# Optimization experiments

Measured on AMD Instinct MI355X. Metric: run time of the kernel, lower is better.

## Reference

```python
import jax, jax.numpy as jnp
import numpy as np
import math

S = 3  # num_subset

def _pe(C, T, V, domain):
    # sinusoidal positional encoding over flattened (T,V) grid -> [1,C,T,V]
    if domain == 'spatial':
        pos = np.tile(np.arange(V), T).astype(np.float32)
    else:
        pos = np.repeat(np.arange(T), V).astype(np.float32)
    div = np.exp(np.arange(0, C, 2).astype(np.float32) * (-math.log(10000.0) / C))
    pe = np.zeros((T * V, C), np.float32)
    pe[:, 0::2] = np.sin(pos[:, None] * div)
    pe[:, 1::2] = np.cos(pos[:, None] * div)
    return jnp.asarray(pe.reshape(T, V, C).transpose(2, 0, 1)[None])

def _conv1(x, W, b):  # 1x1 Conv2d == per-pixel channel matmul
    return jnp.einsum('oc,nctv->notv', W, x) + b[None, :, None, None]

def _bn(x, p):  # eval-mode BatchNorm2d; p: [4,C] = gamma, beta, run_mean, run_var
    g, b, m, v = p
    inv = g / jnp.sqrt(v + 1e-5)
    return (x - m[:, None, None]) * inv[:, None, None] + b[:, None, None]

def _lrelu(x):
    return jnp.where(x > 0, x, 0.1 * x)  # LeakyReLU(0.1)

def _forward(x, Wqk_s, bqk_s, alphas, att0s, Wo_s, bo_s, bn_o_s, Wf_s, bf_s, bn_f_s,
             Wqk_t, bqk_t, alphat, att0t, Wo_t, bo_t, bn_o_t, Wf_t, bf_t, bn_f_t):
    N, C, T, V = x.shape
    R = Wqk_s.shape[0] // (2 * S)  # inter_channels
    # ---- spatial attention (atts buffer is zeros; downs are identity since in==out, stride=1) ----
    y = x + _pe(C, T, V, 'spatial')
    qk = _conv1(y, Wqk_s, bqk_s).reshape(N, 2 * S, R, T, V)
    q, k = qk[:, :S], qk[:, S:]
    att = jnp.tanh(jnp.einsum('nsctu,nsctv->nsuv', q, k) / (R * T)) * alphas + att0s
    y = jnp.einsum('nctu,nsuv->nsctv', x, att).reshape(N, S * C, T, V)
    y = _lrelu(x + _bn(_conv1(y, Wo_s, bo_s), bn_o_s))      # out_nets + residual
    y = _lrelu(x + _bn(_conv1(y, Wf_s, bf_s), bn_f_s))      # ff_nets  + residual
    # ---- temporal attention (attt buffer is zeros; downt are identity) ----
    z = y + _pe(C, T, V, 'temporal')
    qk = _conv1(z, Wqk_t, bqk_t).reshape(N, 2 * S, R, T, V)
    q, k = qk[:, :S], qk[:, S:]
    att = jnp.tanh(jnp.einsum('nsctv,nscqv->nstq', q, k) / (R * V)) * alphat + att0t
    z = jnp.einsum('nctv,nstq->nscqv', y, att).reshape(N, S * C, T, V)
    z = _lrelu(y + _bn(_conv1(z, Wo_t, bo_t), bn_o_t))      # out_nett + residual
    z = _lrelu(y + _bn(_conv1(z, Wf_t, bf_t), bn_f_t))      # ff_nett  + residual
    return z

def setup_inputs() -> dict:
    key = jax.random.key(0)
    ks = jax.random.split(key, 12)
    N, C, T, V, R = 128, 128, 64, 25, 32
    def w(k, o, i):
        return jax.random.normal(k, (o, i), jnp.float32) * np.float32(np.sqrt(2.0 / i))
    def bnp(k, c):
        k1, k2, k3 = jax.random.split(k, 3)
        return jnp.stack([1.0 + 0.1 * jax.random.normal(k1, (c,)),
                          0.1 * jax.random.normal(k2, (c,)),
                          0.1 * jax.random.normal(k3, (c,)),
                          jnp.ones((c,))])
    return {
        'x': jax.random.normal(ks[0], (N, C, T, V), jnp.float32),
        'Wqk_s': w(ks[1], 2 * S * R, C), 'bqk_s': jnp.zeros((2 * S * R,), jnp.float32),
        'alphas': jnp.ones((1, S, 1, 1), jnp.float32),
        'att0s': jnp.ones((1, S, V, V), jnp.float32) / V,
        'Wo_s': w(ks[2], C, S * C), 'bo_s': jnp.zeros((C,), jnp.float32), 'bn_o_s': bnp(ks[3], C),
        'Wf_s': w(ks[4], C, C), 'bf_s': jnp.zeros((C,), jnp.float32), 'bn_f_s': bnp(ks[5], C),
        'Wqk_t': w(ks[6], 2 * S * R, C), 'bqk_t': jnp.zeros((2 * S * R,), jnp.float32),
        'alphat': jnp.ones((1, S, 1, 1), jnp.float32),
        'att0t': jnp.broadcast_to(jnp.eye(T, dtype=jnp.float32), (1, S, T, T)).copy(),
        'Wo_t': w(ks[7], C, S * C), 'bo_t': jnp.zeros((C,), jnp.float32), 'bn_o_t': bnp(ks[8], C),
        'Wf_t': w(ks[9], C, C), 'bf_t': jnp.zeros((C,), jnp.float32), 'bn_f_t': bnp(ks[10], C),
    }

def reference(x, Wqk_s, bqk_s, alphas, att0s, Wo_s, bo_s, bn_o_s, Wf_s, bf_s, bn_f_s,
              Wqk_t, bqk_t, alphat, att0t, Wo_t, bo_t, bn_o_t, Wf_t, bf_t, bn_f_t):
    return _forward(x, Wqk_s, bqk_s, alphas, att0s, Wo_s, bo_s, bn_o_s, Wf_s, bf_s, bn_f_s,
                    Wqk_t, bqk_t, alphat, att0t, Wo_t, bo_t, bn_o_t, Wf_t, bf_t, bn_f_t)
```

## Files before the change

kernel.cpp:

```cpp
#include <hip/hip_runtime.h>
#include <math.h>


typedef __attribute__((ext_vector_type(8))) short short8v;
typedef __attribute__((ext_vector_type(4))) float f32x4;

__device__ __forceinline__ ushort f2bf(float f) {
    uint b = __float_as_uint(f);
    uint r = b + 0x7fffu + ((b >> 16) & 1u);
    return (ushort)(r >> 16);
}
__device__ __forceinline__ float bf2f(ushort h) {
    return __uint_as_float(((uint)h) << 16);
}

__global__ __launch_bounds__(256) void wt_prep(
    const float* __restrict__ Wo_s, const float* __restrict__ Wf_s,
    const float* __restrict__ Wo_t, const float* __restrict__ Wf_t,
    const float* __restrict__ Wqk_s, const float* __restrict__ Wqk_t,
    ushort* __restrict__ W16)
{
    int idx = blockIdx.x * 256 + threadIdx.x;
    if (idx >= 180224) return;
    float v;
    if (idx < 49152) {
        int s = idx / 16384, rem = idx % 16384, o = rem / 128, c = rem % 128;
        v = Wo_s[o * 384 + s * 128 + c];
    } else if (idx < 65536) {
        v = Wf_s[idx - 49152];
    } else if (idx < 114688) {
        int i = idx - 65536, s = i / 16384, rem = i % 16384, o = rem / 128, c = rem % 128;
        v = Wo_t[o * 384 + s * 128 + c];
    } else if (idx < 131072) {
        v = Wf_t[idx - 114688];
    } else if (idx < 155648) {
        v = Wqk_s[idx - 131072];
    } else {
        v = Wqk_t[idx - 155648];
    }
    W16[idx] = f2bf(v);
}

__global__ __launch_bounds__(256) void qk_pe_mfma(
    const float* __restrict__ src, const ushort* __restrict__ Wbf,
    const float* __restrict__ bias, ushort* __restrict__ out)
{
    __shared__ __align__(16) ushort xT[160 * 136];
    __shared__ __align__(16) ushort exch[192 * 24];
    const int n = blockIdx.y, tvb = blockIdx.x * 160;
    const float* sn = src + (size_t)n * 204800;
    for (int i = threadIdx.x; i < 2560; i += 256) {
        int tv4 = (i & 7) + (i >> 9) * 8;
        int cp  = (i >> 3) & 63;
        float4 a = *(const float4*)(sn + (2 * cp) * 1600 + tvb + tv4 * 4);
        float4 b = *(const float4*)(sn + (2 * cp + 1) * 1600 + tvb + tv4 * 4);
        float dv = __expf(-0.14391156831212787f * (float)cp);
        float av[4] = { a.x, a.y, a.z, a.w };
        float bv[4] = { b.x, b.y, b.z, b.w };
#pragma unroll
        for (int e = 0; e < 4; e++) {
            int tv = tvb + tv4 * 4 + e;
            int tt = tv / 25;
            float pos = (float)(tv - tt * 25);
            float ang = pos * dv;
            uint p = (uint)f2bf(av[e] + __sinf(ang)) | ((uint)f2bf(bv[e] + __cosf(ang)) << 16);
            ((uint*)xT)[(tv4 * 4 + e) * 68 + cp] = p;
        }
    }
    __syncthreads();
    const int lane = threadIdx.x & 63, wave = threadIdx.x >> 6;
    const int l15 = lane & 15, kg = lane >> 4;
    const int rb = wave * 48;
    short8v wf[3][4];
#pragma unroll
    for (int nt = 0; nt < 3; nt++)
#pragma unroll
        for (int k = 0; k < 4; k++)
            wf[nt][k] = *(const short8v*)&Wbf[(rb + nt * 16 + l15) * 128 + k * 32 + kg * 8];
    float bsv[3];
#pragma unroll
    for (int nt = 0; nt < 3; nt++) bsv[nt] = bias[rb + nt * 16 + l15];
    ushort* on = out + (size_t)n * 307200;
    for (int mt = 0; mt < 10; mt++) {
        short8v af[4];
#pragma unroll
        for (int k = 0; k < 4; k++)
            af[k] = *(short8v*)&xT[(mt * 16 + l15) * 136 + k * 32 + kg * 8];
        f32x4 accs[3];
#pragma unroll
        for (int nt = 0; nt < 3; nt++) {
            f32x4 acc = {0.f, 0.f, 0.f, 0.f};
#pragma unroll
            for (int k = 0; k < 4; k++)
                acc = __builtin_amdgcn_mfma_f32_16x16x32_bf16(af[k], wf[nt][k], acc, 0, 0, 0);
            accs[nt] = acc;
        }
        __syncthreads();
#pragma unroll
        for (int nt = 0; nt < 3; nt++) {
            uint2 pk;
            pk.x = (uint)f2bf(accs[nt][0] + bsv[nt]) | ((uint)f2bf(accs[nt][1] + bsv[nt]) << 16);
            pk.y = (uint)f2bf(accs[nt][2] + bsv[nt]) | ((uint)f2bf(accs[nt][3] + bsv[nt]) << 16);
            *(uint2*)&exch[(rb + nt * 16 + l15) * 24 + kg * 4] = pk;
        }
        __syncthreads();
        for (int i = threadIdx.x; i < 384; i += 256) {
            int r = i >> 1, hh = i & 1;
            *(uint4*)(on + (size_t)r * 1600 + tvb + mt * 16 + hh * 8) =
                *(const uint4*)&exch[r * 24 + hh * 8];
        }
    }
}

__global__ __launch_bounds__(256) void qk_pe_bf(
    const ushort* __restrict__ ybf, const ushort* __restrict__ Wbf,
    const float* __restrict__ bias, ushort* __restrict__ out)
{
    __shared__ __align__(16) ushort xT[160 * 136];
    __shared__ __align__(16) ushort exch[192 * 24];
    const int n = blockIdx.y, tvb = blockIdx.x * 160;
    const ushort* yq = ybf + (size_t)n * 204800;
    for (int i = threadIdx.x; i < 10240; i += 256) {
        int tv = i >> 6, cp = i & 63;
        uint w = *(const uint*)(yq + (size_t)(tvb + tv) * 128 + cp * 2);
        int t = (tvb + tv) / 25;
        float dv = __expf(-0.14391156831212787f * (float)cp);
        float ang = (float)t * dv;
        float lo = bf2f((ushort)(w & 0xffffu)) + __sinf(ang);
        float hi = bf2f((ushort)(w >> 16)) + __cosf(ang);
        ((uint*)xT)[tv * 68 + cp] = (uint)f2bf(lo) | ((uint)f2bf(hi) << 16);
    }
    __syncthreads();
    const int lane = threadIdx.x & 63, wave = threadIdx.x >> 6;
    const int l15 = lane & 15, kg = lane >> 4;
    const int rb = wave * 48;
    short8v wf[3][4];
#pragma unroll
    for (int nt = 0; nt < 3; nt++)
#pragma unroll
        for (int k = 0; k < 4; k++)
            wf[nt][k] = *(const short8v*)&Wbf[(rb + nt * 16 + l15) * 128 + k * 32 + kg * 8];
    float bsv[3];
#pragma unroll
    for (int nt = 0; nt < 3; nt++) bsv[nt] = bias[rb + nt * 16 + l15];
    ushort* on = out + (size_t)n * 307200;
    for (int mt = 0; mt < 10; mt++) {
        short8v af[4];
#pragma unroll
        for (int k = 0; k < 4; k++)
            af[k] = *(short8v*)&xT[(mt * 16 + l15) * 136 + k * 32 + kg * 8];
        f32x4 accs[3];
#pragma unroll
        for (int nt = 0; nt < 3; nt++) {
            f32x4 acc = {0.f, 0.f, 0.f, 0.f};
#pragma unroll
            for (int k = 0; k < 4; k++)
                acc = __builtin_amdgcn_mfma_f32_16x16x32_bf16(af[k], wf[nt][k], acc, 0, 0, 0);
            accs[nt] = acc;
        }
        __syncthreads();
#pragma unroll
        for (int nt = 0; nt < 3; nt++) {
            uint2 pk;
            pk.x = (uint)f2bf(accs[nt][0] + bsv[nt]) | ((uint)f2bf(accs[nt][1] + bsv[nt]) << 16);
            pk.y = (uint)f2bf(accs[nt][2] + bsv[nt]) | ((uint)f2bf(accs[nt][3] + bsv[nt]) << 16);
            *(uint2*)&exch[(rb + nt * 16 + l15) * 24 + kg * 4] = pk;
        }
        __syncthreads();
        for (int i = threadIdx.x; i < 384; i += 256) {
            int r = i >> 1, hh = i & 1;
            *(uint4*)(on + (size_t)r * 1600 + tvb + mt * 16 + hh * 8) =
                *(const uint4*)&exch[r * 24 + hh * 8];
        }
    }
}

__global__ __launch_bounds__(256) void att_s_mfma(
    const ushort* __restrict__ qk, const float* __restrict__ alphas,
    const float* __restrict__ att0, ushort* __restrict__ attS_bf)
{
    __shared__ __align__(16) ushort Qs[32 * 520];
    __shared__ __align__(16) ushort Ks[32 * 520];
    const int s = blockIdx.x, n = blockIdx.y;
    const ushort* qb = qk + (size_t)n * 307200 + (size_t)(s * 32) * 1600;
    const ushort* kb = qb + 96 * 1600;
    for (int i = threadIdx.x; i < 3072; i += 256) {
        int v = i / 96, k = i - v * 96;
        if (v >= 25 || (k & 31) >= 25) attS_bf[(size_t)n * 3072 + i] = 0;
    }
    const int lane = threadIdx.x & 63, wave = threadIdx.x >> 6;
    const int l15 = lane & 15, kg = lane >> 4;
    const int mt = wave >> 1, nt = wave & 1;
    f32x4 acc = {0.f, 0.f, 0.f, 0.f};
    for (int rc = 0; rc < 4; rc++) {
        __syncthreads();
        for (int i = threadIdx.x; i < 6400; i += 256) {
            int rl = i / 800, j = i - rl * 800;
            uint uq = *(const uint*)(qb + (rc * 8 + rl) * 1600 + j * 2);
            uint uk = *(const uint*)(kb + (rc * 8 + rl) * 1600 + j * 2);
            int tv = j * 2;
            int t0 = tv / 25, u0 = tv - t0 * 25;
            int t1 = (tv + 1) / 25, u1 = (tv + 1) - t1 * 25;
            Qs[u0 * 520 + rl * 64 + t0] = (ushort)(uq & 0xffffu);
            Qs[u1 * 520 + rl * 64 + t1] = (ushort)(uq >> 16);
            Ks[u0 * 520 + rl * 64 + t0] = (ushort)(uk & 0xffffu);
            Ks[u1 * 520 + rl * 64 + t1] = (ushort)(uk >> 16);
        }
        __syncthreads();
#pragma unroll
        for (int ks = 0; ks < 16; ks++) {
            short8v a = *(const short8v*)&Qs[(mt * 16 + l15) * 520 + ks * 32 + kg * 8];
            short8v b = *(const short8v*)&Ks[(nt * 16 + l15) * 520 + ks * 32 + kg * 8];
            acc = __builtin_amdgcn_mfma_f32_16x16x32_bf16(a, b, acc, 0, 0, 0);
        }
    }
    float alpha = alphas[s];
#pragma unroll
    for (int rr = 0; rr < 4; rr++) {
        int u = mt * 16 + kg * 4 + rr, v = nt * 16 + l15;
        if (u < 25 && v < 25)
            attS_bf[(size_t)n * 3072 + v * 96 + s * 32 + u] =
                f2bf(tanhf(acc[rr] * (1.0f / 2048.0f)) * alpha + att0[s * 625 + u * 25 + v]);
    }
}

__global__ __launch_bounds__(256) void att_t_mfma(
    const ushort* __restrict__ qk, const float* __restrict__ alphat,
    const float* __restrict__ att0, ushort* __restrict__ attT_bf)
{
    __shared__ __align__(16) ushort Qt[8 * 64 * 40];
    __shared__ __align__(16) ushort Kt[8 * 64 * 40];
    const int s = blockIdx.x, n = blockIdx.y;
    const ushort* qb = qk + (size_t)n * 307200 + (size_t)(s * 32) * 1600;
    const ushort* kb = qb + 96 * 1600;
    for (int i = threadIdx.x; i < 10240; i += 256) {
        ((uint*)Qt)[i] = 0u;
        ((uint*)Kt)[i] = 0u;
    }
    const int lane = threadIdx.x & 63, wave = threadIdx.x >> 6;
    const int l15 = lane & 15, kg = lane >> 4;
    const int mt = wave;
    f32x4 acc[4];
#pragma unroll
    for (int i = 0; i < 4; i++) acc[i] = (f32x4){0.f, 0.f, 0.f, 0.f};
    for (int rc = 0; rc < 4; rc++) {
        __syncthreads();
        for (int i = threadIdx.x; i < 6400; i += 256) {
            int rl = i / 800, j = i - rl * 800;
            uint uq = *(const uint*)(qb + (rc * 8 + rl) * 1600 + j * 2);
            uint uk = *(const uint*)(kb + (rc * 8 + rl) * 1600 + j * 2);
            int tv = j * 2;
            int t0 = tv / 25, v0 = tv - t0 * 25;
            int t1 = (tv + 1) / 25, v1 = (tv + 1) - t1 * 25;
            Qt[(rl * 64 + t0) * 40 + v0] = (ushort)(uq & 0xffffu);
            Qt[(rl * 64 + t1) * 40 + v1] = (ushort)(uq >> 16);
            Kt[(rl * 64 + t0) * 40 + v0] = (ushort)(uk & 0xffffu);
            Kt[(rl * 64 + t1) * 40 + v1] = (ushort)(uk >> 16);
        }
        __syncthreads();
#pragma unroll
        for (int rl = 0; rl < 8; rl++) {
            short8v a = *(const short8v*)&Qt[(rl * 64 + mt * 16 + l15) * 40 + kg * 8];
#pragma unroll
            for (int nq = 0; nq < 4; nq++) {
                short8v b = *(const short8v*)&Kt[(rl * 64 + nq * 16 + l15) * 40 + kg * 8];
                acc[nq] = __builtin_amdgcn_mfma_f32_16x16x32_bf16(a, b, acc[nq], 0, 0, 0);
            }
        }
    }
    float alpha = alphat[s];
#pragma unroll
    for (int nq = 0; nq < 4; nq++) {
        int q = nq * 16 + l15;
        ushort w4[4];
#pragma unroll
        for (int rr = 0; rr < 4; rr++) {
            int t = mt * 16 + kg * 4 + rr;
            w4[rr] = f2bf(tanhf(acc[nq][rr] * (1.0f / 800.0f)) * alpha +
                          att0[s * 4096 + t * 64 + q]);
        }
        uint2 pk;
        pk.x = (uint)w4[0] | ((uint)w4[1] << 16);
        pk.y = (uint)w4[2] | ((uint)w4[3] << 16);
        *(uint2*)(attT_bf + (size_t)n * 12288 + q * 192 + s * 64 + mt * 16 + kg * 4) = pk;
    }
}

__global__ __launch_bounds__(256) void s_fused(
    const float* __restrict__ x, const ushort* __restrict__ Wo ,
    const ushort* __restrict__ attS , const ushort* __restrict__ Wf,
    const float* __restrict__ bnO, const float* __restrict__ boO,
    const float* __restrict__ bnF, const float* __restrict__ bfF,
    ushort* __restrict__ ybf)
{
    __shared__ __align__(16) ushort xT[64 * 136];
    __shared__ __align__(16) ushort uni[64 * 136];
    __shared__ float sc1[128], of1[128], sc2[128], of2[128];
    const int n = blockIdx.y, tb = blockIdx.x;
    const int tvg0 = tb * 50;
    if (threadIdx.x < 128) {
        int o = threadIdx.x;
        float s1 = bnO[o] * rsqrtf(bnO[384 + o] + 1e-5f);
        sc1[o] = s1; of1[o] = (boO[o] - bnO[256 + o]) * s1 + bnO[128 + o];
    } else {
        int o = threadIdx.x - 128;
        float s2 = bnF[o] * rsqrtf(bnF[384 + o] + 1e-5f);
        sc2[o] = s2; of2[o] = (bfF[o] - bnF[256 + o]) * s2 + bnF[128 + o];
    }
    ushort* Bt = uni;
    for (int i = threadIdx.x; i < 1792; i += 256) {
        int nr = i / 7, k = 25 + i % 7;
        Bt[nr * 32 + (((k >> 3) ^ ((nr >> 1) & 3)) << 3) + (k & 7)] = 0;
    }
    const float* xn = x + (size_t)n * 204800;
    for (int i = threadIdx.x; i < 3200; i += 256) {
        int c = i / 25, j2 = i - c * 25;
        float2 v2 = *(const float2*)(xn + c * 1600 + tvg0 + j2 * 2);
        xT[(j2 * 2) * 136 + c]     = f2bf(v2.x);
        xT[(j2 * 2 + 1) * 136 + c] = f2bf(v2.y);
    }
    __syncthreads();
    const int lane = threadIdx.x & 63, wave = threadIdx.x >> 6;
    const int l15 = lane & 15, kg = lane >> 4;
    const int ob = wave * 32, jb = wave * 4;
    f32x4 accS[2][4];
#pragma unroll
    for (int mt = 0; mt < 2; mt++)
#pragma unroll
        for (int jj = 0; jj < 4; jj++) accS[mt][jj] = (f32x4){0.f, 0.f, 0.f, 0.f};
    const ushort* An = attS + (size_t)n * 3072;
    for (int s = 0; s < 3; s++) {
        short8v bW[2][4];
#pragma unroll
        for (int ot = 0; ot < 2; ot++)
#pragma unroll
            for (int k = 0; k < 4; k++)
                bW[ot][k] = *(const short8v*)&Wo[s * 16384 +
                             (ob + ot * 16 + l15) * 128 + k * 32 + kg * 8];
#pragma unroll
        for (int tt = 0; tt < 4; tt++) {
            short8v aX[4];
#pragma unroll
            for (int k = 0; k < 4; k++)
                aX[k] = *(short8v*)&xT[(tt * 16 + l15) * 136 + k * 32 + kg * 8];
            f32x4 h0 = {0.f, 0.f, 0.f, 0.f}, h1 = {0.f, 0.f, 0.f, 0.f};
#pragma unroll
            for (int k = 0; k < 4; k++) {
                h0 = __builtin_amdgcn_mfma_f32_16x16x32_bf16(aX[k], bW[0][k], h0, 0, 0, 0);
                h1 = __builtin_amdgcn_mfma_f32_16x16x32_bf16(aX[k], bW[1][k], h1, 0, 0, 0);
            }
#pragma unroll
            for (int rr = 0; rr < 4; rr++) {
                int tv = tt * 16 + kg * 4 + rr;
                if (tv < 50) {
                    int tl = tv >= 25 ? 1 : 0, u = tv - tl * 25;
                    int n0 = tl * 128 + ob + l15;
                    int n1 = n0 + 16;
                    Bt[n0 * 32 + (((u >> 3) ^ ((n0 >> 1) & 3)) << 3) + (u & 7)] = f2bf(h0[rr]);
                    Bt[n1 * 32 + (((u >> 3) ^ ((n1 >> 1) & 3)) << 3) + (u & 7)] = f2bf(h1[rr]);
                }
            }
        }
        __syncthreads();
        short8v aA[2];
#pragma unroll
        for (int mt = 0; mt < 2; mt++)
            aA[mt] = *(const short8v*)(An + (mt * 16 + l15) * 96 + s * 32 + kg * 8);
#pragma unroll
        for (int jj = 0; jj < 4; jj++) {
            int nr = (jb + jj) * 16 + l15;
            short8v b = *(const short8v*)&Bt[nr * 32 + ((kg ^ ((nr >> 1) & 3)) << 3)];
#pragma unroll
            for (int mt = 0; mt < 2; mt++)
                accS[mt][jj] = __builtin_amdgcn_mfma_f32_16x16x32_bf16(aA[mt], b, accS[mt][jj], 0, 0, 0);
        }
        __syncthreads();
    }
#pragma unroll
    for (int mt = 0; mt < 2; mt++)
#pragma unroll
        for (int jj = 0; jj < 4; jj++) {
            int nr = (jb + jj) * 16 + l15;
            int tl = nr >> 7, o = nr & 127;
            float sc = sc1[o], of = of1[o];
#pragma unroll
            for (int rr = 0; rr < 4; rr++) {
                int v = mt * 16 + kg * 4 + rr;
                if (v < 25) {
                    int tvl = tl * 25 + v;
                    float h = accS[mt][jj][rr] * sc + of + bf2f(xT[tvl * 136 + o]);
                    h = h > 0.f ? h : 0.1f * h;
                    uni[tvl * 136 + o] = f2bf(h);
                }
            }
        }
    __syncthreads();
    short8v aF[2][4];
#pragma unroll
    for (int mt = 0; mt < 2; mt++)
#pragma unroll
        for (int k = 0; k < 4; k++)
            aF[mt][k] = *(const short8v*)&Wf[(ob + mt * 16 + l15) * 128 + k * 32 + kg * 8];
    f32x4 c0s[4], c1s[4];
#pragma unroll
    for (int nt = 0; nt < 4; nt++) {
        short8v bY[4];
#pragma unroll
        for (int k = 0; k < 4; k++)
            bY[k] = *(short8v*)&uni[(nt * 16 + l15) * 136 + k * 32 + kg * 8];
        f32x4 c0 = {0.f, 0.f, 0.f, 0.f}, c1 = {0.f, 0.f, 0.f, 0.f};
#pragma unroll
        for (int k = 0; k < 4; k++) {
            c0 = __builtin_amdgcn_mfma_f32_16x16x32_bf16(aF[0][k], bY[k], c0, 0, 0, 0);
            c1 = __builtin_amdgcn_mfma_f32_16x16x32_bf16(aF[1][k], bY[k], c1, 0, 0, 0);
        }
        c0s[nt] = c0; c1s[nt] = c1;
    }
    __syncthreads();
#pragma unroll
    for (int nt = 0; nt < 4; nt++) {
        int tv = nt * 16 + l15;
#pragma unroll
        for (int rr = 0; rr < 4; rr++) {
            {
                int o = ob + kg * 4 + rr;
                float h = c0s[nt][rr] * sc2[o] + of2[o] + bf2f(xT[tv * 136 + o]);
                uni[tv * 136 + o] = f2bf(h > 0.f ? h : 0.1f * h);
            }
            {
                int o = ob + 16 + kg * 4 + rr;
                float h = c1s[nt][rr] * sc2[o] + of2[o] + bf2f(xT[tv * 136 + o]);
                uni[tv * 136 + o] = f2bf(h > 0.f ? h : 0.1f * h);
            }
        }
    }
    __syncthreads();
    uint* dst = (uint*)(ybf + (size_t)n * 204800 + (size_t)tvg0 * 128);
    for (int i = threadIdx.x; i < 3200; i += 256) {
        int tv = i >> 6, cp = i & 63;
        dst[tv * 64 + cp] = ((const uint*)uni)[tv * 68 + cp];
    }
}

__global__ __launch_bounds__(256) void t_fused(
    ushort* __restrict__ ybuf ,
    const ushort* __restrict__ Wo ,
    const ushort* __restrict__ Wf ,
    const ushort* __restrict__ attT ,
    const float* __restrict__ bn1, const float* __restrict__ bo1,
    const float* __restrict__ bn2, const float* __restrict__ bf2v)
{
    __shared__ __align__(16) ushort yS[64 * 136];
    __shared__ __align__(16) ushort uni[128 * 72];
    __shared__ float sc1[128], of1[128], sc2[128], of2[128];
    const int v = blockIdx.x, np = blockIdx.y;
    if (threadIdx.x < 128) {
        int o = threadIdx.x;
        float sc = bn1[o] * rsqrtf(bn1[384 + o] + 1e-5f);
        sc1[o] = sc;
        of1[o] = (bo1[o] - bn1[256 + o]) * sc + bn1[128 + o];
    } else {
        int o = threadIdx.x - 128;
        float sc = bn2[o] * rsqrtf(bn2[384 + o] + 1e-5f);
        sc2[o] = sc;
        of2[o] = (bf2v[o] - bn2[256 + o]) * sc + bn2[128 + o];
    }
    ushort* yq = ybuf + (size_t)np * 204800;
    for (int i = threadIdx.x; i < 4096; i += 256) {
        int t = i >> 6, cp = i & 63;
        ((uint*)yS)[t * 68 + cp] = *(const uint*)(yq + (size_t)(t * 25 + v) * 128 + cp * 2);
    }
    __syncthreads();
    const int lane = threadIdx.x & 63, wave = threadIdx.x >> 6;
    const int l15 = lane & 15, kg = lane >> 4;
    const int ob = wave * 32;
    const ushort* An = attT + (size_t)np * 12288;
    ushort* Gl = uni;
    f32x4 acc[4][2];
#pragma unroll
    for (int mt = 0; mt < 4; mt++)
#pragma unroll
        for (int jj = 0; jj < 2; jj++) acc[mt][jj] = (f32x4){0.f, 0.f, 0.f, 0.f};
    for (int s = 0; s < 3; s++) {
        short8v bW[2][4];
#pragma unroll
        for (int nt = 0; nt < 2; nt++)
#pragma unroll
            for (int k = 0; k < 4; k++)
                bW[nt][k] = *(const short8v*)&Wo[s * 16384 +
                             (ob + nt * 16 + l15) * 128 + k * 32 + kg * 8];
#pragma unroll
        for (int mt = 0; mt < 4; mt++) {
            short8v aX[4];
#pragma unroll
            for (int k = 0; k < 4; k++)
                aX[k] = *(short8v*)&yS[(mt * 16 + l15) * 136 + k * 32 + kg * 8];
            f32x4 g0 = {0.f, 0.f, 0.f, 0.f}, g1 = {0.f, 0.f, 0.f, 0.f};
#pragma unroll
            for (int k = 0; k < 4; k++) {
                g0 = __builtin_amdgcn_mfma_f32_16x16x32_bf16(aX[k], bW[0][k], g0, 0, 0, 0);
                g1 = __builtin_amdgcn_mfma_f32_16x16x32_bf16(aX[k], bW[1][k], g1, 0, 0, 0);
            }
#pragma unroll
            for (int rr = 0; rr < 4; rr++) {
                int t = mt * 16 + kg * 4 + rr;
                Gl[(ob + l15) * 72 + t]      = f2bf(g0[rr]);
                Gl[(ob + 16 + l15) * 72 + t] = f2bf(g1[rr]);
            }
        }
        __syncthreads();
#pragma unroll
        for (int ks = 0; ks < 2; ks++) {
            short8v b2[2];
#pragma unroll
            for (int jj = 0; jj < 2; jj++)
                b2[jj] = *(short8v*)&Gl[(ob + jj * 16 + l15) * 72 + ks * 32 + kg * 8];
#pragma unroll
            for (int mt = 0; mt < 4; mt++) {
                short8v a2 = *(const short8v*)(An + (mt * 16 + l15) * 192 + s * 64 + ks * 32 + kg * 8);
#pragma unroll
                for (int jj = 0; jj < 2; jj++)
                    acc[mt][jj] = __builtin_amdgcn_mfma_f32_16x16x32_bf16(a2, b2[jj], acc[mt][jj], 0, 0, 0);
            }
        }
        __syncthreads();
    }
#pragma unroll
    for (int mt = 0; mt < 4; mt++)
#pragma unroll
        for (int jj = 0; jj < 2; jj++) {
            int o = ob + jj * 16 + l15;
            float sc = sc1[o], of = of1[o];
#pragma unroll
            for (int rr = 0; rr < 4; rr++) {
                int q = mt * 16 + kg * 4 + rr;
                float h = acc[mt][jj][rr] * sc + of + bf2f(yS[q * 136 + o]);
                h = h > 0.f ? h : 0.1f * h;
                uni[q * 136 + o] = f2bf(h);
            }
        }
    __syncthreads();
    short8v aF[2][4];
#pragma unroll
    for (int ot = 0; ot < 2; ot++)
#pragma unroll
        for (int k = 0; k < 4; k++)
            aF[ot][k] = *(const short8v*)&Wf[(ob + ot * 16 + l15) * 128 + k * 32 + kg * 8];
    f32x4 c0s[4], c1s[4];
#pragma unroll
    for (int qt = 0; qt < 4; qt++) {
        short8v bY[4];
#pragma unroll
        for (int k = 0; k < 4; k++)
            bY[k] = *(short8v*)&uni[(qt * 16 + l15) * 136 + k * 32 + kg * 8];
        f32x4 c0 = {0.f, 0.f, 0.f, 0.f}, c1 = {0.f, 0.f, 0.f, 0.f};
#pragma unroll
        for (int k = 0; k < 4; k++) {
            c0 = __builtin_amdgcn_mfma_f32_16x16x32_bf16(aF[0][k], bY[k], c0, 0, 0, 0);
            c1 = __builtin_amdgcn_mfma_f32_16x16x32_bf16(aF[1][k], bY[k], c1, 0, 0, 0);
        }
        c0s[qt] = c0; c1s[qt] = c1;
    }
    __syncthreads();
#pragma unroll
    for (int qt = 0; qt < 4; qt++) {
        int q = qt * 16 + l15;
#pragma unroll
        for (int rr = 0; rr < 4; rr++) {
            {
                int o = ob + kg * 4 + rr;
                float h = c0s[qt][rr] * sc2[o] + of2[o] + bf2f(yS[q * 136 + o]);
                uni[q * 136 + o] = f2bf(h > 0.f ? h : 0.1f * h);
            }
            {
                int o = ob + 16 + kg * 4 + rr;
                float h = c1s[qt][rr] * sc2[o] + of2[o] + bf2f(yS[q * 136 + o]);
                uni[q * 136 + o] = f2bf(h > 0.f ? h : 0.1f * h);
            }
        }
    }
    __syncthreads();
    for (int i = threadIdx.x; i < 4096; i += 256) {
        int q = i >> 6, cp = i & 63;
        *(uint*)(yq + (size_t)(q * 25 + v) * 128 + cp * 2) = ((const uint*)uni)[q * 68 + cp];
    }
}

__global__ __launch_bounds__(256) void z_out(
    const ushort* __restrict__ zbf, float* __restrict__ outp)
{
    __shared__ __align__(16) ushort xT[160 * 140];
    const int np = blockIdx.y, tvb = blockIdx.x * 160;
    const ushort* pp = zbf + (size_t)np * 204800 + (size_t)tvb * 128;
    for (int i = threadIdx.x; i < 10240; i += 256) {
        int tv = i >> 6, cp = i & 63;
        ((uint*)xT)[tv * 70 + cp] = *(const uint*)(pp + tv * 128 + cp * 2);
    }
    __syncthreads();
    float* on = outp + (size_t)np * 204800;
    for (int i = threadIdx.x; i < 5120; i += 256) {
        int c = i / 40, w4 = i - c * 40;
        float4 o4;
        o4.x = bf2f(xT[(w4 * 4 + 0) * 140 + c]);
        o4.y = bf2f(xT[(w4 * 4 + 1) * 140 + c]);
        o4.z = bf2f(xT[(w4 * 4 + 2) * 140 + c]);
        o4.w = bf2f(xT[(w4 * 4 + 3) * 140 + c]);
        *(float4*)(on + (size_t)c * 1600 + tvb + w4 * 4) = o4;
    }
}

extern "C" void kernel_launch(void* const* d_in, const int* in_sizes, int n_in,
                              void* d_out, int out_size, void* d_ws, size_t ws_size,
                              hipStream_t stream)
{
    (void)in_sizes; (void)n_in; (void)out_size; (void)ws_size;
    const float* x      = (const float*)d_in[0];
    const float* Wqk_s  = (const float*)d_in[1];
    const float* bqk_s  = (const float*)d_in[2];
    const float* alphas = (const float*)d_in[3];
    const float* att0s  = (const float*)d_in[4];
    const float* Wo_s   = (const float*)d_in[5];
    const float* bo_s   = (const float*)d_in[6];
    const float* bn_o_s = (const float*)d_in[7];
    const float* Wf_s   = (const float*)d_in[8];
    const float* bf_s   = (const float*)d_in[9];
    const float* bn_f_s = (const float*)d_in[10];
    const float* Wqk_t  = (const float*)d_in[11];
    const float* bqk_t  = (const float*)d_in[12];
    const float* alphat = (const float*)d_in[13];
    const float* att0t  = (const float*)d_in[14];
    const float* Wo_t   = (const float*)d_in[15];
    const float* bo_t   = (const float*)d_in[16];
    const float* bn_o_t = (const float*)d_in[17];
    const float* Wf_t   = (const float*)d_in[18];
    const float* bf_t   = (const float*)d_in[19];
    const float* bn_f_t = (const float*)d_in[20];

    float* out = (float*)d_out;
    ushort* qk_d    = (ushort*)d_out;
    ushort* ybf     = (ushort*)d_ws;
    ushort* attS_bf = (ushort*)((char*)d_ws + 78643200);
    ushort* attT_bf = (ushort*)((char*)d_ws + 79603200);
    ushort* W16     = (ushort*)((char*)d_ws + 85894656);
    const ushort* WoS_bf  = W16;
    const ushort* WfS_bf  = W16 + 49152;
    const ushort* WoT_bf  = W16 + 65536;
    const ushort* WfT_bf  = W16 + 114688;
    const ushort* WqkS_bf = W16 + 131072;
    const ushort* WqkT_bf = W16 + 155648;

    wt_prep<<<704, 256, 0, stream>>>(Wo_s, Wf_s, Wo_t, Wf_t, Wqk_s, Wqk_t, W16);

    dim3 gqk(10, 128), gatt(3, 128), gsf(32, 128), gtf(25, 128), gzo(10, 128);

    qk_pe_mfma<<<gqk, 256, 0, stream>>>(x, WqkS_bf, bqk_s, qk_d);
    att_s_mfma<<<gatt, 256, 0, stream>>>(qk_d, alphas, att0s, attS_bf);
    s_fused<<<gsf, 256, 0, stream>>>(x, WoS_bf, attS_bf, WfS_bf,
                                     bn_o_s, bo_s, bn_f_s, bf_s, ybf);

    qk_pe_bf<<<gqk, 256, 0, stream>>>(ybf, WqkT_bf, bqk_t, qk_d);
    att_t_mfma<<<gatt, 256, 0, stream>>>(qk_d, alphat, att0t, attT_bf);
    t_fused<<<gtf, 256, 0, stream>>>(ybf, WoT_bf, WfT_bf, attT_bf,
                                     bn_o_t, bo_t, bn_f_t, bf_t);
    z_out<<<gzo, 256, 0, stream>>>(ybf, out);
}
```

Measured before the change: 417.9 us.

## Convert x to channel-last bf16 once and reuse it for spatial QK and s_fused

```diff
diff --git a/kernel.cpp b/kernel.cpp
--- a/kernel.cpp
+++ b/kernel.cpp
@@ -41,91 +41,49 @@
     W16[idx] = f2bf(v);
 }
 
-__global__ __launch_bounds__(256) void qk_pe_mfma(
-    const float* __restrict__ src, const ushort* __restrict__ Wbf,
-    const float* __restrict__ bias, ushort* __restrict__ out)
+__global__ __launch_bounds__(256) void x_cvt(
+    const float* __restrict__ x, ushort* __restrict__ xbf)
 {
     __shared__ __align__(16) ushort xT[160 * 136];
-    __shared__ __align__(16) ushort exch[192 * 24];
-    const int n = blockIdx.y, tvb = blockIdx.x * 160;
-    const float* sn = src + (size_t)n * 204800;
+    const int np = blockIdx.y, tvb = blockIdx.x * 160;
+    const float* sn = x + (size_t)np * 204800;
     for (int i = threadIdx.x; i < 2560; i += 256) {
         int tv4 = (i & 7) + (i >> 9) * 8;
         int cp  = (i >> 3) & 63;
         float4 a = *(const float4*)(sn + (2 * cp) * 1600 + tvb + tv4 * 4);
         float4 b = *(const float4*)(sn + (2 * cp + 1) * 1600 + tvb + tv4 * 4);
-        float dv = __expf(-0.14391156831212787f * (float)cp);
         float av[4] = { a.x, a.y, a.z, a.w };
         float bv[4] = { b.x, b.y, b.z, b.w };
 #pragma unroll
         for (int e = 0; e < 4; e++) {
-            int tv = tvb + tv4 * 4 + e;
-            int tt = tv / 25;
-            float pos = (float)(tv - tt * 25);
-            float ang = pos * dv;
-            uint p = (uint)f2bf(av[e] + __sinf(ang)) | ((uint)f2bf(bv[e] + __cosf(ang)) << 16);
+            uint p = (uint)f2bf(av[e]) | ((uint)f2bf(bv[e]) << 16);
             ((uint*)xT)[(tv4 * 4 + e) * 68 + cp] = p;
         }
     }
     __syncthreads();
-    const int lane = threadIdx.x & 63, wave = threadIdx.x >> 6;
-    const int l15 = lane & 15, kg = lane >> 4;
-    const int rb = wave * 48;
-    short8v wf[3][4];
-#pragma unroll
-    for (int nt = 0; nt < 3; nt++)
-#pragma unroll
-        for (int k = 0; k < 4; k++)
-            wf[nt][k] = *(const short8v*)&Wbf[(rb + nt * 16 + l15) * 128 + k * 32 + kg * 8];
-    float bsv[3];
-#pragma unroll
-    for (int nt = 0; nt < 3; nt++) bsv[nt] = bias[rb + nt * 16 + l15];
-    ushort* on = out + (size_t)n * 307200;
-    for (int mt = 0; mt < 10; mt++) {
-        short8v af[4];
-#pragma unroll
-        for (int k = 0; k < 4; k++)
-            af[k] = *(short8v*)&xT[(mt * 16 + l15) * 136 + k * 32 + kg * 8];
-        f32x4 accs[3];
-#pragma unroll
-        for (int nt = 0; nt < 3; nt++) {
-            f32x4 acc = {0.f, 0.f, 0.f, 0.f};
-#pragma unroll
-            for (int k = 0; k < 4; k++)
-                acc = __builtin_amdgcn_mfma_f32_16x16x32_bf16(af[k], wf[nt][k], acc, 0, 0, 0);
-            accs[nt] = acc;
-        }
-        __syncthreads();
-#pragma unroll
-        for (int nt = 0; nt < 3; nt++) {
-            uint2 pk;
-            pk.x = (uint)f2bf(accs[nt][0] + bsv[nt]) | ((uint)f2bf(accs[nt][1] + bsv[nt]) << 16);
-            pk.y = (uint)f2bf(accs[nt][2] + bsv[nt]) | ((uint)f2bf(accs[nt][3] + bsv[nt]) << 16);
-            *(uint2*)&exch[(rb + nt * 16 + l15) * 24 + kg * 4] = pk;
-        }
-        __syncthreads();
-        for (int i = threadIdx.x; i < 384; i += 256) {
-            int r = i >> 1, hh = i & 1;
-            *(uint4*)(on + (size_t)r * 1600 + tvb + mt * 16 + hh * 8) =
-                *(const uint4*)&exch[r * 24 + hh * 8];
-        }
+    uint* dst = (uint*)(xbf + (size_t)np * 204800 + (size_t)tvb * 128);
+    for (int i = threadIdx.x; i < 10240; i += 256) {
+        int tv = i >> 6, cp = i & 63;
+        dst[tv * 64 + cp] = ((const uint*)xT)[tv * 68 + cp];
     }
 }
 
 __global__ __launch_bounds__(256) void qk_pe_bf(
-    const ushort* __restrict__ ybf, const ushort* __restrict__ Wbf,
-    const float* __restrict__ bias, ushort* __restrict__ out)
+    const ushort* __restrict__ src, const ushort* __restrict__ Wbf,
+    const float* __restrict__ bias, ushort* __restrict__ out, int pos_is_t)
 {
     __shared__ __align__(16) ushort xT[160 * 136];
     __shared__ __align__(16) ushort exch[192 * 24];
     const int n = blockIdx.y, tvb = blockIdx.x * 160;
-    const ushort* yq = ybf + (size_t)n * 204800;
+    const ushort* yq = src + (size_t)n * 204800;
     for (int i = threadIdx.x; i < 10240; i += 256) {
         int tv = i >> 6, cp = i & 63;
         uint w = *(const uint*)(yq + (size_t)(tvb + tv) * 128 + cp * 2);
-        int t = (tvb + tv) / 25;
+        int tvg = tvb + tv;
+        int t = tvg / 25;
+        float pos = pos_is_t ? (float)t : (float)(tvg - t * 25);
         float dv = __expf(-0.14391156831212787f * (float)cp);
-        float ang = (float)t * dv;
+        float ang = pos * dv;
         float lo = bf2f((ushort)(w & 0xffffu)) + __sinf(ang);
         float hi = bf2f((ushort)(w >> 16)) + __cosf(ang);
         ((uint*)xT)[tv * 68 + cp] = (uint)f2bf(lo) | ((uint)f2bf(hi) << 16);
@@ -287,14 +245,14 @@
 }
 
 __global__ __launch_bounds__(256) void s_fused(
-    const float* __restrict__ x, const ushort* __restrict__ Wo ,
+    ushort* __restrict__ xbuf ,
+    const ushort* __restrict__ Wo ,
     const ushort* __restrict__ attS , const ushort* __restrict__ Wf,
     const float* __restrict__ bnO, const float* __restrict__ boO,
-    const float* __restrict__ bnF, const float* __restrict__ bfF,
-    ushort* __restrict__ ybf)
+    const float* __restrict__ bnF, const float* __restrict__ bfF)
 {
     __shared__ __align__(16) ushort xT[64 * 136];
-    __shared__ __align__(16) ushort uni[64 * 136];
+    __shared__ __align__(16) ushort uni[10240];
     __shared__ float sc1[128], of1[128], sc2[128], of2[128];
     const int n = blockIdx.y, tb = blockIdx.x;
     const int tvg0 = tb * 50;
@@ -310,14 +268,12 @@
     ushort* Bt = uni;
     for (int i = threadIdx.x; i < 1792; i += 256) {
         int nr = i / 7, k = 25 + i % 7;
-        Bt[nr * 32 + (((k >> 3) ^ ((nr >> 1) & 3)) << 3) + (k & 7)] = 0;
-    }
-    const float* xn = x + (size_t)n * 204800;
+        Bt[nr * 40 + k] = 0;
+    }
+    ushort* xq = xbuf + (size_t)n * 204800;
     for (int i = threadIdx.x; i < 3200; i += 256) {
-        int c = i / 25, j2 = i - c * 25;
-        float2 v2 = *(const float2*)(xn + c * 1600 + tvg0 + j2 * 2);
-        xT[(j2 * 2) * 136 + c]     = f2bf(v2.x);
-        xT[(j2 * 2 + 1) * 136 + c] = f2bf(v2.y);
+        int tv = i >> 6, cp = i & 63;
+        ((uint*)xT)[tv * 68 + cp] = *(const uint*)(xq + (size_t)(tvg0 + tv) * 128 + cp * 2);
     }
     __syncthreads();
     const int lane = threadIdx.x & 63, wave = threadIdx.x >> 6;
@@ -355,9 +311,8 @@
                 if (tv < 50) {
                     int tl = tv >= 25 ? 1 : 0, u = tv - tl * 25;
                     int n0 = tl * 128 + ob + l15;
-                    int n1 = n0 + 16;
-                    Bt[n0 * 32 + (((u >> 3) ^ ((n0 >> 1) & 3)) << 3) + (u & 7)] = f2bf(h0[rr]);
-                    Bt[n1 * 32 + (((u >> 3) ^ ((n1 >> 1) & 3)) << 3) + (u & 7)] = f2bf(h1[rr]);
+                    Bt[n0 * 40 + u]        = f2bf(h0[rr]);
+                    Bt[(n0 + 16) * 40 + u] = f2bf(h1[rr]);
                 }
             }
         }
@@ -369,7 +324,7 @@
 #pragma unroll
         for (int jj = 0; jj < 4; jj++) {
             int nr = (jb + jj) * 16 + l15;
-            short8v b = *(const short8v*)&Bt[nr * 32 + ((kg ^ ((nr >> 1) & 3)) << 3)];
+            short8v b = *(const short8v*)&Bt[nr * 40 + kg * 8];
 #pragma unroll
             for (int mt = 0; mt < 2; mt++)
                 accS[mt][jj] = __builtin_amdgcn_mfma_f32_16x16x32_bf16(aA[mt], b, accS[mt][jj], 0, 0, 0);
@@ -435,10 +390,9 @@
         }
     }
     __syncthreads();
-    uint* dst = (uint*)(ybf + (size_t)n * 204800 + (size_t)tvg0 * 128);
     for (int i = threadIdx.x; i < 3200; i += 256) {
         int tv = i >> 6, cp = i & 63;
-        dst[tv * 64 + cp] = ((const uint*)uni)[tv * 68 + cp];
+        *(uint*)(xq + (size_t)(tvg0 + tv) * 128 + cp * 2) = ((const uint*)uni)[tv * 68 + cp];
     }
 }
 
@@ -638,7 +592,7 @@
 
     float* out = (float*)d_out;
     ushort* qk_d    = (ushort*)d_out;
-    ushort* ybf     = (ushort*)d_ws;
+    ushort* xybuf   = (ushort*)d_ws;
     ushort* attS_bf = (ushort*)((char*)d_ws + 78643200);
     ushort* attT_bf = (ushort*)((char*)d_ws + 79603200);
     ushort* W16     = (ushort*)((char*)d_ws + 85894656);
@@ -651,16 +605,17 @@
 
     wt_prep<<<704, 256, 0, stream>>>(Wo_s, Wf_s, Wo_t, Wf_t, Wqk_s, Wqk_t, W16);
 
-    dim3 gqk(10, 128), gatt(3, 128), gsf(32, 128), gtf(25, 128), gzo(10, 128);
-
-    qk_pe_mfma<<<gqk, 256, 0, stream>>>(x, WqkS_bf, bqk_s, qk_d);
+    dim3 gqk(10, 128), gatt(3, 128), gsf(32, 128), gtf(25, 128), gcv(10, 128);
+
+    x_cvt<<<gcv, 256, 0, stream>>>(x, xybuf);
+    qk_pe_bf<<<gqk, 256, 0, stream>>>(xybuf, WqkS_bf, bqk_s, qk_d, 0);
     att_s_mfma<<<gatt, 256, 0, stream>>>(qk_d, alphas, att0s, attS_bf);
-    s_fused<<<gsf, 256, 0, stream>>>(x, WoS_bf, attS_bf, WfS_bf,
-                                     bn_o_s, bo_s, bn_f_s, bf_s, ybf);
-
-    qk_pe_bf<<<gqk, 256, 0, stream>>>(ybf, WqkT_bf, bqk_t, qk_d);
+    s_fused<<<gsf, 256, 0, stream>>>(xybuf, WoS_bf, attS_bf, WfS_bf,
+                                     bn_o_s, bo_s, bn_f_s, bf_s);
+
+    qk_pe_bf<<<gqk, 256, 0, stream>>>(xybuf, WqkT_bf, bqk_t, qk_d, 1);
     att_t_mfma<<<gatt, 256, 0, stream>>>(qk_d, alphat, att0t, attT_bf);
-    t_fused<<<gtf, 256, 0, stream>>>(ybf, WoT_bf, WfT_bf, attT_bf,
+    t_fused<<<gtf, 256, 0, stream>>>(xybuf, WoT_bf, WfT_bf, attT_bf,
                                      bn_o_t, bo_t, bn_f_t, bf_t);
-    z_out<<<gzo, 256, 0, stream>>>(ybf, out);
-}
+    z_out<<<gtf.x == 25 ? dim3(10, 128) : dim3(10, 128), 256, 0, stream>>>(xybuf, out);
+}
```

Result: no change. 425.3 us (+1.8%).
